# Kernel tuning notes

Hardware: AMD Instinct MI355X
Metric: run time of the kernel (lower is better)

## Reference

```python
import jax, jax.numpy as jnp
import numpy as np

T, B, OBS, A, P, NB, H = 32, 256, 1024, 16, 600, 601, 128


def setup_inputs() -> dict:
    key = jax.random.key(0)
    ks = jax.random.split(key, 32)
    f32 = jnp.float32

    def rn(k, shape, scale):
        return jax.random.normal(k, shape, dtype=f32) * scale

    hh = 1.0 / np.sqrt(H)
    inp = {
        "obs_seq": rn(ks[0], (T, B, OBS), 1.0),
        # backbone MLP (512, 512)
        "bb_w1": rn(ks[1], (OBS, 512), 1.0 / np.sqrt(OBS)), "bb_b1": jnp.zeros((512,), f32),
        "bb_w2": rn(ks[2], (512, 512), 1.0 / np.sqrt(512)), "bb_b2": jnp.zeros((512,), f32),
        # feedforward heads (final layers init std=0.01, bias 0 per module)
        "pol_w": rn(ks[3], (512, A), 0.01), "pol_b": jnp.zeros((A,), f32),
        "y_w": rn(ks[4], (512, P), 0.01), "y_b": jnp.zeros((P,), f32),
        "ci_w": rn(ks[5], (512, H), 1.0 / np.sqrt(512)), "ci_b": jnp.zeros((H,), f32),
        # LSTMCell(A, 128): gate order i,f,g,o as in torch
        "w_ih": rn(ks[6], (A, 4 * H), hh), "w_hh": rn(ks[7], (H, 4 * H), hh),
        "b_ih": rn(ks[8], (4 * H,), hh), "b_hh": rn(ks[9], (4 * H,), hh),
        # z / q / aux_pi MLPs: Linear(128,128) -> ReLU -> Linear(128, out)
        "z_w1": rn(ks[10], (H, H), hh), "z_b1": jnp.zeros((H,), f32),
        "z_w2": rn(ks[11], (H, P), 0.01), "z_b2": jnp.zeros((P,), f32),
        "q_w1": rn(ks[12], (H, H), hh), "q_b1": jnp.zeros((H,), f32),
        "q_w2": rn(ks[13], (H, NB), 0.01), "q_b2": jnp.zeros((NB,), f32),
        "a_w1": rn(ks[14], (H, H), hh), "a_b1": jnp.zeros((H,), f32),
        "a_w2": rn(ks[15], (H, A), 0.01), "a_b2": jnp.zeros((A,), f32),
    }
    return inp


def reference(obs_seq, bb_w1, bb_b1, bb_w2, bb_b2, pol_w, pol_b, y_w, y_b,
              ci_w, ci_b, w_ih, w_hh, b_ih, b_hh,
              z_w1, z_b1, z_w2, z_b2, q_w1, q_b1, q_w2, q_b2,
              a_w1, a_b1, a_w2, a_b2):
    Tn, Bn = obs_seq.shape[:2]
    x = obs_seq.reshape(Tn * Bn, -1)  # feedforward across time: fold T into batch
    emb = jax.nn.relu(jax.nn.relu(x @ bb_w1 + bb_b1) @ bb_w2 + bb_b2)  # [N,512]
    logits = emb @ pol_w + pol_b  # [N,A]
    y = emb @ y_w + y_b           # [N,P]
    c0 = emb @ ci_w + ci_b        # [N,H]
    h0 = jnp.tanh(c0)

    # one_hot(a) @ W_ih^T == row a of W_ih (input-to-gate contribution per action)
    in_gates = w_ih + b_ih  # [A, 4H]

    def step(carry, ig):
        h, c = carry
        g = ig + h @ w_hh + b_hh  # [N,4H]
        i, f, gg, o = jnp.split(g, 4, axis=-1)  # torch gate order i,f,g,o
        c = jax.nn.sigmoid(f) * c + jax.nn.sigmoid(i) * jnp.tanh(gg)
        h = jax.nn.sigmoid(o) * jnp.tanh(c)
        return (h, c), h

    _, h_all = jax.lax.scan(step, (h0, c0), in_gates)  # [A, N, H]

    def mlp(hx, w1, b1, w2, b2):
        return jax.nn.relu(hx @ w1 + b1) @ w2 + b2

    def to_tba(arr):
        Aa, N, D = arr.shape
        return arr.reshape(Aa, Tn, Bn, D).transpose(1, 2, 0, 3)  # [T,B,A,D]

    z = to_tba(mlp(h_all, z_w1, z_b1, z_w2, z_b2))
    q = to_tba(mlp(h_all, q_w1, q_b1, q_w2, q_b2))
    aux_pi = to_tba(mlp(h_all, a_w1, a_b1, a_w2, a_b2))
    return (logits.reshape(Tn, Bn, -1), y.reshape(Tn, Bn, -1), z, q, aux_pi)
```

## Files before the change

kernel.cpp:

```cpp
#include <hip/hip_runtime.h>
#include <stdint.h>

typedef short bf16x8 __attribute__((ext_vector_type(8)));
typedef float f32x4 __attribute__((ext_vector_type(4)));

__device__ __forceinline__ unsigned short f2b(float f) {
  union { float f; unsigned u; } v; v.f = f;
  unsigned r = v.u + 0x7fffu + ((v.u >> 16) & 1u);
  return (unsigned short)(r >> 16);
}

__global__ __launch_bounds__(256) void tconv(const float* __restrict__ in,
                                             unsigned short* __restrict__ out,
                                             int R, int C) {
  __shared__ float t[32][33];
  int c0 = blockIdx.x * 32, r0 = blockIdx.y * 32;
  int tx = threadIdx.x & 31, ty = threadIdx.x >> 5;
  #pragma unroll
  for (int i = 0; i < 32; i += 8) {
    int r = r0 + ty + i, c = c0 + tx;
    t[ty + i][tx] = (r < R && c < C) ? in[(size_t)r * C + c] : 0.f;
  }
  __syncthreads();
  #pragma unroll
  for (int i = 0; i < 32; i += 8) {
    int c = c0 + ty + i, r = r0 + tx;
    if (c < C && r < R) out[(size_t)c * R + r] = f2b(t[tx][ty + i]);
  }
}

template <int ACT, bool AF32, bool OBF16>
__global__ __launch_bounds__(256) void gemm_k(const void* __restrict__ Ap,
                                              const unsigned short* __restrict__ BT,
                                              const float* __restrict__ bias,
                                              void* __restrict__ Cp,
                                              int M, int N, int K, int ldC) {
  __shared__ unsigned short As[64][40];
  __shared__ unsigned short Bs[64][40];
  const int tid = threadIdx.x;
  const int n0 = blockIdx.x * 64;
  const int m0 = blockIdx.y * 64;
  const int wid = tid >> 6, lane = tid & 63;
  const int wm = (wid >> 1) * 32, wn = (wid & 1) * 32;
  const int lr = lane & 15, lk = lane >> 4;
  const int sr = tid >> 2, sc = (tid & 3) * 8;

  f32x4 acc[2][2] = {};

  for (int k0 = 0; k0 < K; k0 += 32) {
    if (AF32) {
      const float* A = (const float*)Ap;
      const float* p = A + (size_t)(m0 + sr) * K + k0 + sc;
      float4 f0 = *(const float4*)p;
      float4 f1 = *(const float4*)(p + 4);
      bf16x8 v;
      v[0] = (short)f2b(f0.x); v[1] = (short)f2b(f0.y);
      v[2] = (short)f2b(f0.z); v[3] = (short)f2b(f0.w);
      v[4] = (short)f2b(f1.x); v[5] = (short)f2b(f1.y);
      v[6] = (short)f2b(f1.z); v[7] = (short)f2b(f1.w);
      *(bf16x8*)&As[sr][sc] = v;
    } else {
      const unsigned short* A = (const unsigned short*)Ap;
      *(bf16x8*)&As[sr][sc] = *(const bf16x8*)(A + (size_t)(m0 + sr) * K + k0 + sc);
    }
    {
      int n = n0 + sr;
      bf16x8 v = {};
      if (n < N) v = *(const bf16x8*)(BT + (size_t)n * K + k0 + sc);
      *(bf16x8*)&Bs[sr][sc] = v;
    }
    __syncthreads();
    bf16x8 af[2], bfr[2];
    #pragma unroll
    for (int mi = 0; mi < 2; mi++) af[mi] = *(const bf16x8*)&As[wm + mi * 16 + lr][lk * 8];
    #pragma unroll
    for (int ni = 0; ni < 2; ni++) bfr[ni] = *(const bf16x8*)&Bs[wn + ni * 16 + lr][lk * 8];
    #pragma unroll
    for (int mi = 0; mi < 2; mi++)
      #pragma unroll
      for (int ni = 0; ni < 2; ni++)
        acc[mi][ni] = __builtin_amdgcn_mfma_f32_16x16x32_bf16(af[mi], bfr[ni], acc[mi][ni], 0, 0, 0);
    __syncthreads();
  }

  #pragma unroll
  for (int mi = 0; mi < 2; mi++)
    #pragma unroll
    for (int ni = 0; ni < 2; ni++) {
      int col = n0 + wn + ni * 16 + lr;
      if (col >= N) continue;
      float bv = bias[col];
      #pragma unroll
      for (int r = 0; r < 4; r++) {
        int row = m0 + wm + mi * 16 + lk * 4 + r;
        float v = acc[mi][ni][r] + bv;
        if (ACT == 1) v = fmaxf(v, 0.f);
        if (OBF16) ((unsigned short*)Cp)[(size_t)row * ldC + col] = f2b(v);
        else       ((float*)Cp)[(size_t)row * ldC + col] = v;
      }
    }
}

__global__ __launch_bounds__(256) void lstm_k(const float* __restrict__ c0,
                                              const unsigned short* __restrict__ whhT,
                                              const float* __restrict__ w_ih,
                                              const float* __restrict__ b_ih,
                                              const float* __restrict__ b_hh,
                                              unsigned short* __restrict__ h_all) {
  __shared__ float G[32][516];
  __shared__ float cst[32][128];
  __shared__ unsigned short hst[32][136];
  const int tid = threadIdx.x, lane = tid & 63, wid = tid >> 6;
  const int r0 = blockIdx.x * 32;
  const int lr = lane & 15, lk = lane >> 4;

  for (int e = tid; e < 32 * 128; e += 256) {
    int r = e >> 7, j = e & 127;
    float c = c0[(size_t)(r0 + r) * 128 + j];
    cst[r][j] = c;
    hst[r][j] = f2b(tanhf(c));
  }
  __syncthreads();

  for (int a = 0; a < 16; a++) {
    f32x4 acc[2][8] = {};
    #pragma unroll
    for (int ks = 0; ks < 4; ks++) {
      bf16x8 af0 = *(const bf16x8*)&hst[lr][ks * 32 + lk * 8];
      bf16x8 af1 = *(const bf16x8*)&hst[16 + lr][ks * 32 + lk * 8];
      #pragma unroll
      for (int ni = 0; ni < 8; ni++) {
        int col = wid * 128 + ni * 16 + lr;
        bf16x8 bv = *(const bf16x8*)(whhT + (size_t)col * 128 + ks * 32 + lk * 8);
        acc[0][ni] = __builtin_amdgcn_mfma_f32_16x16x32_bf16(af0, bv, acc[0][ni], 0, 0, 0);
        acc[1][ni] = __builtin_amdgcn_mfma_f32_16x16x32_bf16(af1, bv, acc[1][ni], 0, 0, 0);
      }
    }
    #pragma unroll
    for (int mi = 0; mi < 2; mi++)
      #pragma unroll
      for (int ni = 0; ni < 8; ni++)
        #pragma unroll
        for (int rr = 0; rr < 4; rr++)
          G[mi * 16 + lk * 4 + rr][wid * 128 + ni * 16 + lr] = acc[mi][ni][rr];
    __syncthreads();

    const float* ig = w_ih + a * 512;
    for (int e = tid; e < 32 * 128; e += 256) {
      int r = e >> 7, j = e & 127;
      float gi = G[r][j]       + ig[j]       + b_ih[j]       + b_hh[j];
      float gf = G[r][j + 128] + ig[j + 128] + b_ih[j + 128] + b_hh[j + 128];
      float gg = G[r][j + 256] + ig[j + 256] + b_ih[j + 256] + b_hh[j + 256];
      float go = G[r][j + 384] + ig[j + 384] + b_ih[j + 384] + b_hh[j + 384];
      float c = cst[r][j];
      float si = 1.f / (1.f + __expf(-gi));
      float sf = 1.f / (1.f + __expf(-gf));
      float so = 1.f / (1.f + __expf(-go));
      float cn = sf * c + si * tanhf(gg);
      float h = so * tanhf(cn);
      cst[r][j] = cn;
      unsigned short hb = f2b(h);
      hst[r][j] = hb;
      h_all[((size_t)(r0 + r) * 16 + a) * 128 + j] = hb;
    }
    __syncthreads();
  }
}

extern "C" void kernel_launch(void* const* d_in, const int* in_sizes, int n_in,
                              void* d_out, int out_size, void* d_ws, size_t ws_size,
                              hipStream_t stream) {
  const float* obs   = (const float*)d_in[0];
  const float* bb_w1 = (const float*)d_in[1];
  const float* bb_b1 = (const float*)d_in[2];
  const float* bb_w2 = (const float*)d_in[3];
  const float* bb_b2 = (const float*)d_in[4];
  const float* pol_w = (const float*)d_in[5];
  const float* pol_b = (const float*)d_in[6];
  const float* y_w   = (const float*)d_in[7];
  const float* y_b   = (const float*)d_in[8];
  const float* ci_w  = (const float*)d_in[9];
  const float* ci_b  = (const float*)d_in[10];
  const float* w_ih  = (const float*)d_in[11];
  const float* w_hh  = (const float*)d_in[12];
  const float* b_ih  = (const float*)d_in[13];
  const float* b_hh  = (const float*)d_in[14];
  const float* z_w1  = (const float*)d_in[15];
  const float* z_b1  = (const float*)d_in[16];
  const float* z_w2  = (const float*)d_in[17];
  const float* z_b2  = (const float*)d_in[18];
  const float* q_w1  = (const float*)d_in[19];
  const float* q_b1  = (const float*)d_in[20];
  const float* q_w2  = (const float*)d_in[21];
  const float* q_b2  = (const float*)d_in[22];
  const float* a_w1  = (const float*)d_in[23];
  const float* a_b1  = (const float*)d_in[24];
  const float* a_w2  = (const float*)d_in[25];
  const float* a_b2  = (const float*)d_in[26];

  float* out = (float*)d_out;
  float* out_logits = out;
  float* out_y      = out + 131072;
  float* out_z      = out + 5046272;
  float* out_q      = out + 83689472;
  float* out_a      = out + 162463744;

  uint8_t* ws = (uint8_t*)d_ws;
  size_t off = 0;
  auto alc = [&](size_t bytes) -> void* {
    void* p = ws + off;
    off = (off + bytes + 255) & ~(size_t)255;
    return p;
  };
  unsigned short* W1T  = (unsigned short*)alc((size_t)512 * 1024 * 2);
  unsigned short* W2T  = (unsigned short*)alc((size_t)512 * 512 * 2);
  unsigned short* polT = (unsigned short*)alc((size_t)16 * 512 * 2);
  unsigned short* yT   = (unsigned short*)alc((size_t)600 * 512 * 2);
  unsigned short* ciT  = (unsigned short*)alc((size_t)128 * 512 * 2);
  unsigned short* whhT = (unsigned short*)alc((size_t)512 * 128 * 2);
  unsigned short* zw1T = (unsigned short*)alc((size_t)128 * 128 * 2);
  unsigned short* zw2T = (unsigned short*)alc((size_t)600 * 128 * 2);
  unsigned short* qw1T = (unsigned short*)alc((size_t)128 * 128 * 2);
  unsigned short* qw2T = (unsigned short*)alc((size_t)601 * 128 * 2);
  unsigned short* aw1T = (unsigned short*)alc((size_t)128 * 128 * 2);
  unsigned short* aw2T = (unsigned short*)alc((size_t)16 * 128 * 2);
  unsigned short* hid1 = (unsigned short*)alc((size_t)8192 * 512 * 2);
  unsigned short* emb  = (unsigned short*)alc((size_t)8192 * 512 * 2);
  float*          c0b  = (float*)alc((size_t)8192 * 128 * 4);
  unsigned short* hall = (unsigned short*)alc((size_t)8192 * 16 * 128 * 2);
  unsigned short* hh   = (unsigned short*)alc((size_t)131072 * 128 * 2);
  (void)ws_size; (void)in_sizes; (void)n_in; (void)out_size;

  dim3 B256(256);
  tconv<<<dim3(16, 32), B256, 0, stream>>>(bb_w1, W1T, 1024, 512);
  tconv<<<dim3(16, 16), B256, 0, stream>>>(bb_w2, W2T, 512, 512);
  tconv<<<dim3(1, 16),  B256, 0, stream>>>(pol_w, polT, 512, 16);
  tconv<<<dim3(19, 16), B256, 0, stream>>>(y_w, yT, 512, 600);
  tconv<<<dim3(4, 16),  B256, 0, stream>>>(ci_w, ciT, 512, 128);
  tconv<<<dim3(16, 4),  B256, 0, stream>>>(w_hh, whhT, 128, 512);
  tconv<<<dim3(4, 4),   B256, 0, stream>>>(z_w1, zw1T, 128, 128);
  tconv<<<dim3(19, 4),  B256, 0, stream>>>(z_w2, zw2T, 128, 600);
  tconv<<<dim3(4, 4),   B256, 0, stream>>>(q_w1, qw1T, 128, 128);
  tconv<<<dim3(19, 4),  B256, 0, stream>>>(q_w2, qw2T, 128, 601);
  tconv<<<dim3(4, 4),   B256, 0, stream>>>(a_w1, aw1T, 128, 128);
  tconv<<<dim3(1, 4),   B256, 0, stream>>>(a_w2, aw2T, 128, 16);

  gemm_k<1, true,  true><<<dim3(8, 128), B256, 0, stream>>>(obs,  W1T, bb_b1, hid1, 8192, 512, 1024, 512);
  gemm_k<1, false, true><<<dim3(8, 128), B256, 0, stream>>>(hid1, W2T, bb_b2, emb,  8192, 512, 512,  512);
  gemm_k<0, false, false><<<dim3(1, 128),  B256, 0, stream>>>(emb, polT, pol_b, out_logits, 8192, 16,  512, 16);
  gemm_k<0, false, false><<<dim3(10, 128), B256, 0, stream>>>(emb, yT,   y_b,   out_y,      8192, 600, 512, 600);
  gemm_k<0, false, false><<<dim3(2, 128),  B256, 0, stream>>>(emb, ciT,  ci_b,  c0b,        8192, 128, 512, 128);
  lstm_k<<<dim3(256), B256, 0, stream>>>(c0b, whhT, w_ih, b_ih, b_hh, hall);
  gemm_k<1, false, true ><<<dim3(2, 2048),  B256, 0, stream>>>(hall, zw1T, z_b1, hh,    131072, 128, 128, 128);
  gemm_k<0, false, false><<<dim3(10, 2048), B256, 0, stream>>>(hh,   zw2T, z_b2, out_z, 131072, 600, 128, 600);
  gemm_k<1, false, true ><<<dim3(2, 2048),  B256, 0, stream>>>(hall, qw1T, q_b1, hh,    131072, 128, 128, 128);
  gemm_k<0, false, false><<<dim3(10, 2048), B256, 0, stream>>>(hh,   qw2T, q_b2, out_q, 131072, 601, 128, 601);
  gemm_k<1, false, true ><<<dim3(2, 2048),  B256, 0, stream>>>(hall, aw1T, a_b1, hh,    131072, 128, 128, 128);
  gemm_k<0, false, false><<<dim3(1, 2048),  B256, 0, stream>>>(hh,   aw2T, a_b2, out_a, 131072, 16,  128, 16);
}
```

Baseline: 590.8 us.

## Fuse z/q/aux head MLPs into one kernel and batch weight transposes

Replaces the six per-head GEMM launches with a single heads_k kernel. Each block loads a 64-row tile of LSTM hidden states into shared memory once, computes the hidden ReLU layer in LDS and writes all three head outputs, so the intermediate hh buffer no longer round-trips through global memory. It also merges the twelve weight-transpose launches into one launch indexed by blockIdx.z. The f32 observation input is now converted to bf16 in a separate pass rather than inside the first GEMM. The fused kernel reads second-layer weights straight from global memory with no LDS staging, and its output stores may be poorly coalesced.

```diff
diff --git a/kernel.cpp b/kernel.cpp
--- a/kernel.cpp
+++ b/kernel.cpp
@@ -10,27 +10,42 @@
   return (unsigned short)(r >> 16);
 }
 
-__global__ __launch_bounds__(256) void tconv(const float* __restrict__ in,
-                                             unsigned short* __restrict__ out,
-                                             int R, int C) {
-  __shared__ float t[32][33];
+struct TD { const float* in; unsigned short* out; int R, C; };
+struct TDs { TD d[12]; };
+
+__global__ __launch_bounds__(256) void tconv_all(TDs ds) {
+  TD t = ds.d[blockIdx.z];
   int c0 = blockIdx.x * 32, r0 = blockIdx.y * 32;
+  if (c0 >= t.C || r0 >= t.R) return;
+  __shared__ float tl[32][33];
   int tx = threadIdx.x & 31, ty = threadIdx.x >> 5;
   #pragma unroll
   for (int i = 0; i < 32; i += 8) {
     int r = r0 + ty + i, c = c0 + tx;
-    t[ty + i][tx] = (r < R && c < C) ? in[(size_t)r * C + c] : 0.f;
+    tl[ty + i][tx] = (r < t.R && c < t.C) ? t.in[(size_t)r * t.C + c] : 0.f;
   }
   __syncthreads();
   #pragma unroll
   for (int i = 0; i < 32; i += 8) {
     int c = c0 + ty + i, r = r0 + tx;
-    if (c < C && r < R) out[(size_t)c * R + r] = f2b(t[tx][ty + i]);
-  }
-}
-
-template <int ACT, bool AF32, bool OBF16>
-__global__ __launch_bounds__(256) void gemm_k(const void* __restrict__ Ap,
+    if (c < t.C && r < t.R) t.out[(size_t)c * t.R + r] = f2b(tl[tx][ty + i]);
+  }
+}
+
+__global__ __launch_bounds__(256) void conv_k(const float* __restrict__ in,
+                                              unsigned short* __restrict__ out, int n) {
+  int i = (blockIdx.x * 256 + threadIdx.x) * 8;
+  if (i >= n) return;
+  float4 a = *(const float4*)(in + i);
+  float4 b = *(const float4*)(in + i + 4);
+  bf16x8 v;
+  v[0] = (short)f2b(a.x); v[1] = (short)f2b(a.y); v[2] = (short)f2b(a.z); v[3] = (short)f2b(a.w);
+  v[4] = (short)f2b(b.x); v[5] = (short)f2b(b.y); v[6] = (short)f2b(b.z); v[7] = (short)f2b(b.w);
+  *(bf16x8*)(out + i) = v;
+}
+
+template <int ACT, bool OBF16>
+__global__ __launch_bounds__(256) void gemm_k(const unsigned short* __restrict__ A,
                                               const unsigned short* __restrict__ BT,
                                               const float* __restrict__ bias,
                                               void* __restrict__ Cp,
@@ -48,21 +63,7 @@
   f32x4 acc[2][2] = {};
 
   for (int k0 = 0; k0 < K; k0 += 32) {
-    if (AF32) {
-      const float* A = (const float*)Ap;
-      const float* p = A + (size_t)(m0 + sr) * K + k0 + sc;
-      float4 f0 = *(const float4*)p;
-      float4 f1 = *(const float4*)(p + 4);
-      bf16x8 v;
-      v[0] = (short)f2b(f0.x); v[1] = (short)f2b(f0.y);
-      v[2] = (short)f2b(f0.z); v[3] = (short)f2b(f0.w);
-      v[4] = (short)f2b(f1.x); v[5] = (short)f2b(f1.y);
-      v[6] = (short)f2b(f1.z); v[7] = (short)f2b(f1.w);
-      *(bf16x8*)&As[sr][sc] = v;
-    } else {
-      const unsigned short* A = (const unsigned short*)Ap;
-      *(bf16x8*)&As[sr][sc] = *(const bf16x8*)(A + (size_t)(m0 + sr) * K + k0 + sc);
-    }
+    *(bf16x8*)&As[sr][sc] = *(const bf16x8*)(A + (size_t)(m0 + sr) * K + k0 + sc);
     {
       int n = n0 + sr;
       bf16x8 v = {};
@@ -162,6 +163,130 @@
       unsigned short hb = f2b(h);
       hst[r][j] = hb;
       h_all[((size_t)(r0 + r) * 16 + a) * 128 + j] = hb;
+    }
+    __syncthreads();
+  }
+}
+
+__global__ __launch_bounds__(256) void heads_k(
+    const unsigned short* __restrict__ hall,
+    const unsigned short* __restrict__ zw1, const float* __restrict__ zb1,
+    const unsigned short* __restrict__ zw2, const float* __restrict__ zb2,
+    const unsigned short* __restrict__ qw1, const float* __restrict__ qb1,
+    const unsigned short* __restrict__ qw2, const float* __restrict__ qb2,
+    const unsigned short* __restrict__ aw1, const float* __restrict__ ab1,
+    const unsigned short* __restrict__ aw2, const float* __restrict__ ab2,
+    float* __restrict__ oz, float* __restrict__ oq, float* __restrict__ oa) {
+  __shared__ unsigned short hs[64][136];
+  __shared__ unsigned short hd[64][136];
+  const int tid = threadIdx.x;
+  const int r0 = blockIdx.x * 64;
+  const int lane = tid & 63, wid = tid >> 6;
+  const int lr = lane & 15, lk = lane >> 4;
+
+  {
+    int row = tid >> 2, cb = (tid & 3) * 8;
+    #pragma unroll
+    for (int it = 0; it < 4; it++) {
+      int col = cb + it * 32;
+      *(bf16x8*)&hs[row][col] = *(const bf16x8*)(hall + (size_t)(r0 + row) * 128 + col);
+    }
+  }
+  __syncthreads();
+
+  const unsigned short* W1[3] = {zw1, qw1, aw1};
+  const float*          B1[3] = {zb1, qb1, ab1};
+  const unsigned short* W2[3] = {zw2, qw2, aw2};
+  const float*          B2[3] = {zb2, qb2, ab2};
+  float*                OO[3] = {oz, oq, oa};
+  const int             NN[3] = {600, 601, 16};
+
+  #pragma unroll
+  for (int hi = 0; hi < 3; hi++) {
+    const unsigned short* w1 = W1[hi];
+    const unsigned short* w2 = W2[hi];
+    const float* b1 = B1[hi];
+    const float* b2 = B2[hi];
+    float* Oh = OO[hi];
+    const int Nh = NN[hi];
+
+    {
+      bf16x8 ha[4][4];
+      #pragma unroll
+      for (int mi = 0; mi < 4; mi++)
+        #pragma unroll
+        for (int ks = 0; ks < 4; ks++)
+          ha[mi][ks] = *(const bf16x8*)&hs[mi * 16 + lr][ks * 32 + lk * 8];
+      f32x4 hacc[4][2] = {};
+      #pragma unroll
+      for (int ks = 0; ks < 4; ks++)
+        #pragma unroll
+        for (int nj = 0; nj < 2; nj++) {
+          int col = wid * 32 + nj * 16 + lr;
+          bf16x8 bv = *(const bf16x8*)(w1 + (size_t)col * 128 + ks * 32 + lk * 8);
+          #pragma unroll
+          for (int mi = 0; mi < 4; mi++)
+            hacc[mi][nj] = __builtin_amdgcn_mfma_f32_16x16x32_bf16(ha[mi][ks], bv, hacc[mi][nj], 0, 0, 0);
+        }
+      #pragma unroll
+      for (int mi = 0; mi < 4; mi++)
+        #pragma unroll
+        for (int nj = 0; nj < 2; nj++) {
+          int col = wid * 32 + nj * 16 + lr;
+          float bb = b1[col];
+          #pragma unroll
+          for (int rr = 0; rr < 4; rr++) {
+            int row = mi * 16 + lk * 4 + rr;
+            hd[row][col] = f2b(fmaxf(hacc[mi][nj][rr] + bb, 0.f));
+          }
+        }
+    }
+    __syncthreads();
+
+    {
+      bf16x8 hda[4][4];
+      #pragma unroll
+      for (int mi = 0; mi < 4; mi++)
+        #pragma unroll
+        for (int ks = 0; ks < 4; ks++)
+          hda[mi][ks] = *(const bf16x8*)&hd[mi * 16 + lr][ks * 32 + lk * 8];
+
+      const int NF = (Nh + 15) >> 4;
+      const int fpw = (NF + 3) >> 2;
+      const int f0 = wid * fpw;
+      const int f1 = min(NF, f0 + fpw);
+
+      for (int f = f0; f < f1; f += 2) {
+        f32x4 oacc[4][2] = {};
+        #pragma unroll
+        for (int ks = 0; ks < 4; ks++)
+          #pragma unroll
+          for (int nj = 0; nj < 2; nj++) {
+            int nf = f + nj; nf = nf < f1 ? nf : f1 - 1;
+            int col = nf * 16 + lr;
+            int bc = col < Nh ? col : Nh - 1;
+            bf16x8 bv = *(const bf16x8*)(w2 + (size_t)bc * 128 + ks * 32 + lk * 8);
+            #pragma unroll
+            for (int mi = 0; mi < 4; mi++)
+              oacc[mi][nj] = __builtin_amdgcn_mfma_f32_16x16x32_bf16(hda[mi][ks], bv, oacc[mi][nj], 0, 0, 0);
+          }
+        #pragma unroll
+        for (int nj = 0; nj < 2; nj++) {
+          int nf = f + nj;
+          if (nf >= f1) break;
+          int col = nf * 16 + lr;
+          if (col < Nh) {
+            float bb = b2[col];
+            #pragma unroll
+            for (int mi = 0; mi < 4; mi++)
+              #pragma unroll
+              for (int rr = 0; rr < 4; rr++) {
+                int row = r0 + mi * 16 + lk * 4 + rr;
+                Oh[(size_t)row * Nh + col] = oacc[mi][nj][rr] + bb;
+              }
+          }
+        }
+      }
     }
     __syncthreads();
   }
@@ -224,37 +349,41 @@
   unsigned short* qw2T = (unsigned short*)alc((size_t)601 * 128 * 2);
   unsigned short* aw1T = (unsigned short*)alc((size_t)128 * 128 * 2);
   unsigned short* aw2T = (unsigned short*)alc((size_t)16 * 128 * 2);
+  unsigned short* obsb = (unsigned short*)alc((size_t)8192 * 1024 * 2);
   unsigned short* hid1 = (unsigned short*)alc((size_t)8192 * 512 * 2);
   unsigned short* emb  = (unsigned short*)alc((size_t)8192 * 512 * 2);
   float*          c0b  = (float*)alc((size_t)8192 * 128 * 4);
   unsigned short* hall = (unsigned short*)alc((size_t)8192 * 16 * 128 * 2);
-  unsigned short* hh   = (unsigned short*)alc((size_t)131072 * 128 * 2);
   (void)ws_size; (void)in_sizes; (void)n_in; (void)out_size;
 
   dim3 B256(256);
-  tconv<<<dim3(16, 32), B256, 0, stream>>>(bb_w1, W1T, 1024, 512);
-  tconv<<<dim3(16, 16), B256, 0, stream>>>(bb_w2, W2T, 512, 512);
-  tconv<<<dim3(1, 16),  B256, 0, stream>>>(pol_w, polT, 512, 16);
-  tconv<<<dim3(19, 16), B256, 0, stream>>>(y_w, yT, 512, 600);
-  tconv<<<dim3(4, 16),  B256, 0, stream>>>(ci_w, ciT, 512, 128);
-  tconv<<<dim3(16, 4),  B256, 0, stream>>>(w_hh, whhT, 128, 512);
-  tconv<<<dim3(4, 4),   B256, 0, stream>>>(z_w1, zw1T, 128, 128);
-  tconv<<<dim3(19, 4),  B256, 0, stream>>>(z_w2, zw2T, 128, 600);
-  tconv<<<dim3(4, 4),   B256, 0, stream>>>(q_w1, qw1T, 128, 128);
-  tconv<<<dim3(19, 4),  B256, 0, stream>>>(q_w2, qw2T, 128, 601);
-  tconv<<<dim3(4, 4),   B256, 0, stream>>>(a_w1, aw1T, 128, 128);
-  tconv<<<dim3(1, 4),   B256, 0, stream>>>(a_w2, aw2T, 128, 16);
-
-  gemm_k<1, true,  true><<<dim3(8, 128), B256, 0, stream>>>(obs,  W1T, bb_b1, hid1, 8192, 512, 1024, 512);
-  gemm_k<1, false, true><<<dim3(8, 128), B256, 0, stream>>>(hid1, W2T, bb_b2, emb,  8192, 512, 512,  512);
-  gemm_k<0, false, false><<<dim3(1, 128),  B256, 0, stream>>>(emb, polT, pol_b, out_logits, 8192, 16,  512, 16);
-  gemm_k<0, false, false><<<dim3(10, 128), B256, 0, stream>>>(emb, yT,   y_b,   out_y,      8192, 600, 512, 600);
-  gemm_k<0, false, false><<<dim3(2, 128),  B256, 0, stream>>>(emb, ciT,  ci_b,  c0b,        8192, 128, 512, 128);
+
+  TDs td;
+  td.d[0]  = {bb_w1, W1T, 1024, 512};
+  td.d[1]  = {bb_w2, W2T, 512, 512};
+  td.d[2]  = {pol_w, polT, 512, 16};
+  td.d[3]  = {y_w,   yT,   512, 600};
+  td.d[4]  = {ci_w,  ciT,  512, 128};
+  td.d[5]  = {w_hh,  whhT, 128, 512};
+  td.d[6]  = {z_w1,  zw1T, 128, 128};
+  td.d[7]  = {z_w2,  zw2T, 128, 600};
+  td.d[8]  = {q_w1,  qw1T, 128, 128};
+  td.d[9]  = {q_w2,  qw2T, 128, 601};
+  td.d[10] = {a_w1,  aw1T, 128, 128};
+  td.d[11] = {a_w2,  aw2T, 128, 16};
+  tconv_all<<<dim3(19, 32, 12), B256, 0, stream>>>(td);
+
+  conv_k<<<dim3(4096), B256, 0, stream>>>(obs, obsb, 8192 * 1024);
+
+  gemm_k<1, true><<<dim3(8, 128), B256, 0, stream>>>(obsb, W1T, bb_b1, hid1, 8192, 512, 1024, 512);
+  gemm_k<1, true><<<dim3(8, 128), B256, 0, stream>>>(hid1, W2T, bb_b2, emb,  8192, 512, 512,  512);
+  gemm_k<0, false><<<dim3(1, 128),  B256, 0, stream>>>(emb, polT, pol_b, out_logits, 8192, 16,  512, 16);
+  gemm_k<0, false><<<dim3(10, 128), B256, 0, stream>>>(emb, yT,   y_b,   out_y,      8192, 600, 512, 600);
+  gemm_k<0, false><<<dim3(2, 128),  B256, 0, stream>>>(emb, ciT,  ci_b,  c0b,        8192, 128, 512, 128);
   lstm_k<<<dim3(256), B256, 0, stream>>>(c0b, whhT, w_ih, b_ih, b_hh, hall);
-  gemm_k<1, false, true ><<<dim3(2, 2048),  B256, 0, stream>>>(hall, zw1T, z_b1, hh,    131072, 128, 128, 128);
-  gemm_k<0, false, false><<<dim3(10, 2048), B256, 0, stream>>>(hh,   zw2T, z_b2, out_z, 131072, 600, 128, 600);
-  gemm_k<1, false, true ><<<dim3(2, 2048),  B256, 0, stream>>>(hall, qw1T, q_b1, hh,    131072, 128, 128, 128);
-  gemm_k<0, false, false><<<dim3(10, 2048), B256, 0, stream>>>(hh,   qw2T, q_b2, out_q, 131072, 601, 128, 601);
-  gemm_k<1, false, true ><<<dim3(2, 2048),  B256, 0, stream>>>(hall, aw1T, a_b1, hh,    131072, 128, 128, 128);
-  gemm_k<0, false, false><<<dim3(1, 2048),  B256, 0, stream>>>(hh,   aw2T, a_b2, out_a, 131072, 16,  128, 16);
-}
+  heads_k<<<dim3(2048), B256, 0, stream>>>(hall,
+                                           zw1T, z_b1, zw2T, z_b2,
+                                           qw1T, q_b1, qw2T, q_b2,
+                                           aw1T, a_b1, aw2T, a_b2,
+                                           out_z, out_q, out_a);
+}
```

After: 523.2 us. 11.4% less time.
